# Kernel tuning notes

Measured on AMD Instinct MI355X. Metric: run time of the kernel, lower is better.

## Reference

```python
import jax, jax.numpy as jnp
import numpy as np

B, CIN, H, W = 32, 256, 32, 32
DK, DV, HEADS, OUT = 128, 128, 8, 256
DKH = DK // HEADS
DVH = DV // HEADS


def _conv1x1(x, w, b):
    # x: [B,C,H,W], w: [O,C], b: [O]
    return jnp.einsum('bchw,oc->bohw', x, w) + b[None, :, None, None]


def setup_inputs() -> dict:
    key = jax.random.key(0)
    ks = jax.random.split(key, 7)
    s = 0.02
    return {
        'x': jax.random.normal(ks[0], (B, CIN, H, W), jnp.float32),
        'w_qkv': jax.random.normal(ks[1], (2 * DK + DV, CIN), jnp.float32) * s,
        'b_qkv': jnp.zeros((2 * DK + DV,), jnp.float32),
        'w_attn': jax.random.normal(ks[2], (DV, DV), jnp.float32) * s,
        'b_attn': jnp.zeros((DV,), jnp.float32),
        'w_out': jax.random.normal(ks[3], (OUT - DV, CIN), jnp.float32) * s,
        'b_out': jnp.zeros((OUT - DV,), jnp.float32),
    }


def reference(x, w_qkv, b_qkv, w_attn, b_attn, w_out, b_out):
    b = x.shape[0]
    N = H * W
    # parallel conv branch (kernel_size=1 so spatial dims match attention branch)
    conv_out = _conv1x1(x, w_out, b_out)  # [B, OUT-DV, H, W]
    # qkv projection
    qkv = _conv1x1(x, w_qkv, b_qkv)  # [B, 2*DK+DV, H, W]
    q, k, v = jnp.split(qkv, [DK, 2 * DK], axis=1)
    q = q.reshape(b, HEADS, DKH, N) * (DKH ** -0.5)
    k = k.reshape(b, HEADS, DKH, N)
    v = v.reshape(b, HEADS, DVH, N)
    # scaled dot-product attention over the N=H*W flattened positions
    logits = jnp.einsum('bhdq,bhdk->bhqk', q, k)  # [B,heads,N,N]
    weights = jax.nn.softmax(logits, axis=-1)
    attn = jnp.einsum('bhqk,bhdk->bhdq', weights, v)  # [B,heads,DVH,N]
    attn = attn.reshape(b, DV, H, W)
    attn = _conv1x1(attn, w_attn, b_attn)
    return jnp.concatenate([conv_out, attn], axis=1)
```

## Files before the change

### kernel.cpp

```cpp
#include <hip/hip_runtime.h>
#include <hip/hip_bf16.h>

#define BATCH 32
#define CIN   256
#define NPOS  1024
#define DKC   128
#define DVC   128
#define HEADS 8
#define OUTC  256

typedef __bf16 bf16x8 __attribute__((ext_vector_type(8)));
typedef __bf16 bf16x4 __attribute__((ext_vector_type(4)));
typedef float  f32x4  __attribute__((ext_vector_type(4)));
typedef float  f32x16 __attribute__((ext_vector_type(16)));
typedef unsigned u32x4 __attribute__((ext_vector_type(4)));
typedef unsigned short u16x8 __attribute__((ext_vector_type(8)));

#define QSCALE 0.3606737602f

__device__ inline bf16x8 load8(const __bf16* p) {
    return *reinterpret_cast<const bf16x8*>(p);
}
__device__ inline f32x4 fzero4() {
    f32x4 z;
#pragma unroll
    for (int i = 0; i < 4; ++i) z[i] = 0.0f;
    return z;
}
__device__ inline float fexp2(float x) {
#if __has_builtin(__builtin_amdgcn_exp2f)
    return __builtin_amdgcn_exp2f(x);
#else
    return exp2f(x);
#endif
}

__global__ __launch_bounds__(1024) void detect_dtype(const unsigned short* __restrict__ xraw,
                                                     int* __restrict__ flag) {
    __shared__ int s;
    if (threadIdx.x == 0) s = 0;
    __syncthreads();
    int cnt = 0;
#pragma unroll
    for (int r = 0; r < 4; ++r) {
        u16x8 v = *reinterpret_cast<const u16x8*>(xraw + ((size_t)r * 1024 + threadIdx.x) * 8);
#pragma unroll
        for (int j = 0; j < 8; ++j) {
            unsigned int e = (v[j] >> 7) & 0xFF;
            if (e >= 0x92) cnt++;
        }
    }
    if (cnt) atomicAdd(&s, cnt);
    __syncthreads();
    if (threadIdx.x == 0) *flag = (s > 0) ? 1 : 0;
}

#define CV_WQKV 98304
#define CV_WOUT (CV_WQKV + 32768)
#define CV_BQKV (CV_WOUT + 384)
#define CV_BOUT (CV_BQKV + 128)
#define CV_WATT (CV_BOUT + 16384)
#define CV_BATT (CV_WATT + 128)
__global__ __launch_bounds__(256) void convert_all(
    const void* __restrict__ w_qkv, const void* __restrict__ b_qkv,
    const void* __restrict__ w_attn, const void* __restrict__ b_attn,
    const void* __restrict__ w_out, const void* __restrict__ b_out,
    __bf16* __restrict__ wcat, __bf16* __restrict__ bcat,
    __bf16* __restrict__ w_attnc, __bf16* __restrict__ b_attnc,
    const int* __restrict__ flag) {
    int i = blockIdx.x * 256 + threadIdx.x;
    const void* src; __bf16* dst; int j;
    if      (i < CV_WQKV) { src = w_qkv;  j = i;           dst = wcat + i; }
    else if (i < CV_WOUT) { src = w_out;  j = i - CV_WQKV; dst = wcat + i; }
    else if (i < CV_BQKV) { src = b_qkv;  j = i - CV_WOUT; dst = bcat + j; }
    else if (i < CV_BOUT) { src = b_out;  j = i - CV_BQKV; dst = bcat + 384 + j; }
    else if (i < CV_WATT) { src = w_attn; j = i - CV_BOUT; dst = w_attnc + j; }
    else if (i < CV_BATT) { src = b_attn; j = i - CV_WATT; dst = b_attnc + j; }
    else return;
    if (*flag) *dst = (__bf16)((const float*)src)[j];
    else       *dst = ((const __bf16*)src)[j];
}

__global__ __launch_bounds__(512, 4) void qkv_conv_gemm3(
    const void* __restrict__ xv,
    const __bf16* __restrict__ wcat,
    const __bf16* __restrict__ bcat,
    __bf16* __restrict__ q_ws,
    __bf16* __restrict__ k_ws,
    __bf16* __restrict__ v_ws,
    void* __restrict__ out,
    const int* __restrict__ flag)
{
    __shared__ __bf16 xs[64][264];
    bool isf32 = (*flag != 0);
    int b   = blockIdx.y;
    int n0  = blockIdx.x * 64;
    int t   = threadIdx.x;
    int nl  = t & 63, cb = t >> 6;

#pragma unroll
    for (int cs = 0; cs < 32; ++cs) {
        int c = cs * 8 + cb;
        size_t gi = ((size_t)b * CIN + c) * NPOS + n0 + nl;
        float v = isf32 ? ((const float*)xv)[gi] : (float)((const __bf16*)xv)[gi];
        xs[nl][c] = (__bf16)v;
    }
    __syncthreads();

    int wave = t >> 6;
    int lane = t & 63;
    int quad = lane >> 4, colid = lane & 15;
    int row0 = (wave >> 2) * 256 + (wave & 3) * 64;

    const __bf16* wp = wcat + (size_t)(row0 + colid) * CIN + quad * 8;

    f32x4 acc[4][4];
#pragma unroll
    for (int rt = 0; rt < 4; ++rt)
#pragma unroll
        for (int st = 0; st < 4; ++st) acc[rt][st] = fzero4();

#pragma unroll
    for (int k0 = 0; k0 < CIN; k0 += 32) {
        bf16x8 aA[4], bB[4];
#pragma unroll
        for (int rt = 0; rt < 4; ++rt)
            aA[rt] = load8(wp + (size_t)(rt * 16) * CIN + k0);
#pragma unroll
        for (int st = 0; st < 4; ++st)
            bB[st] = *reinterpret_cast<const bf16x8*>(&xs[st * 16 + colid][k0 + quad * 8]);
#pragma unroll
        for (int rt = 0; rt < 4; ++rt)
#pragma unroll
            for (int st = 0; st < 4; ++st)
                acc[rt][st] = __builtin_amdgcn_mfma_f32_16x16x32_bf16(aA[rt], bB[st], acc[rt][st], 0, 0, 0);
    }

#pragma unroll
    for (int rt = 0; rt < 4; ++rt) {
        int obase = row0 + rt * 16;
        float bias[4];
#pragma unroll
        for (int r = 0; r < 4; ++r) bias[r] = (float)bcat[obase + quad * 4 + r];

        if (obase < DKC) {
            int h = obase >> 4;
            __bf16* qb = q_ws + (((size_t)b * HEADS + h) * NPOS + n0) * 16 + quad * 4;
#pragma unroll
            for (int st = 0; st < 4; ++st) {
                bf16x4 ov;
#pragma unroll
                for (int r = 0; r < 4; ++r)
                    ov[r] = (__bf16)((acc[rt][st][r] + bias[r]) * QSCALE);
                *reinterpret_cast<bf16x4*>(qb + (size_t)(st * 16 + colid) * 16) = ov;
            }
        } else if (obase < 2 * DKC) {
            int h = (obase - DKC) >> 4;
            __bf16* kb = k_ws + (((size_t)b * HEADS + h) * NPOS + n0) * 16 + quad * 4;
#pragma unroll
            for (int st = 0; st < 4; ++st) {
                bf16x4 ov;
#pragma unroll
                for (int r = 0; r < 4; ++r)
                    ov[r] = (__bf16)(acc[rt][st][r] + bias[r]);
                *reinterpret_cast<bf16x4*>(kb + (size_t)(st * 16 + colid) * 16) = ov;
            }
        } else if (obase < 384) {
            int h = (obase - 2 * DKC) >> 4;
            __bf16* vb = v_ws + (((size_t)b * HEADS + h) * 16 + quad * 4) * NPOS + n0 + colid;
#pragma unroll
            for (int r = 0; r < 4; ++r)
#pragma unroll
                for (int st = 0; st < 4; ++st)
                    vb[(size_t)r * NPOS + st * 16] = (__bf16)(acc[rt][st][r] + bias[r]);
        } else {
            int oc = obase - 384 + quad * 4;
#pragma unroll
            for (int r = 0; r < 4; ++r) {
                size_t ob = ((size_t)b * OUTC + oc + r) * NPOS + n0 + colid;
#pragma unroll
                for (int st = 0; st < 4; ++st) {
                    float v = acc[rt][st][r] + bias[r];
                    if (isf32) __builtin_nontemporal_store(v, (float*)out + ob + st * 16);
                    else       __builtin_nontemporal_store((__bf16)v, (__bf16*)out + ob + st * 16);
                }
            }
        }
    }
}

#define OSTR 136
__global__ __launch_bounds__(512, 4) void attention_kernel(
    const __bf16* __restrict__ q_ws,
    const __bf16* __restrict__ k_ws,
    const __bf16* __restrict__ v_ws,
    const __bf16* __restrict__ w_attn,
    const __bf16* __restrict__ b_attn,
    void* __restrict__ out,
    const int* __restrict__ flag)
{
    __shared__ __align__(16) __bf16 olds[64][OSTR];
    int b    = blockIdx.x;
    int nq0  = blockIdx.y * 64;
    int wave = threadIdx.x >> 6;
    int lane = threadIdx.x & 63;
    int l5   = lane & 31, hi = lane >> 5;
    int h    = wave;
    int bh   = b * HEADS + h;

    const __bf16* qp = q_ws + (size_t)bh * NPOS * 16;
    const __bf16* kp = k_ws + (size_t)bh * NPOS * 16;
    const __bf16* vp = v_ws + (size_t)bh * 16 * NPOS;

    bf16x8 qB0 = load8(qp + (size_t)(nq0 + l5) * 16 + hi * 8);
    bf16x8 qB1 = load8(qp + (size_t)(nq0 + 32 + l5) * 16 + hi * 8);

    bf16x8 vA0, vA1;
#pragma unroll
    for (int i = 0; i < 8; ++i) { vA0[i] = (__bf16)1.0f; vA1[i] = (__bf16)1.0f; }
    const __bf16* vrow = vp + (size_t)l5 * NPOS + hi * 8;

    f32x16 zero16;
#pragma unroll
    for (int i = 0; i < 16; ++i) zero16[i] = 0.0f;
    f32x16 acc0 = zero16, acc1 = zero16;

    bf16x8 kA = load8(kp + (size_t)l5 * 16 + hi * 8);
    if (l5 < 16) {
        vA0 = load8(vrow);
        vA1 = load8(vrow + 16);
    }

#pragma unroll 2
    for (int nk0 = 0; nk0 < NPOS; nk0 += 32) {
        int nkn = (nk0 + 32) & (NPOS - 1);
        bf16x8 kA_n = load8(kp + (size_t)(nkn + l5) * 16 + hi * 8);
        bf16x8 vA0_n = vA0, vA1_n = vA1;
        if (l5 < 16) {
            vA0_n = load8(vrow + nkn);
            vA1_n = load8(vrow + nkn + 16);
        }
#pragma unroll
        for (int half = 0; half < 2; ++half) {
            f32x16 st = __builtin_amdgcn_mfma_f32_32x32x16_bf16(
                kA, half ? qB1 : qB0, zero16, 0, 0, 0);
            unsigned w[8];
#pragma unroll
            for (int m = 0; m < 4; ++m) {
                float e0 = fexp2(st[4 * m + 0]);
                float e1 = fexp2(st[4 * m + 1]);
                float e2 = fexp2(st[4 * m + 2]);
                float e3 = fexp2(st[4 * m + 3]);
                unsigned lo, hw;
                asm("v_cvt_pk_bf16_f32 %0, %1, %2" : "=v"(lo) : "v"(e0), "v"(e1));
                asm("v_cvt_pk_bf16_f32 %0, %1, %2" : "=v"(hw) : "v"(e2), "v"(e3));
                w[2 * m]     = lo;
                w[2 * m + 1] = hw;
            }
            asm("v_permlane32_swap_b32 %0, %1" : "+v"(w[0]), "+v"(w[2]));
            asm("v_permlane32_swap_b32 %0, %1" : "+v"(w[1]), "+v"(w[3]));
            asm("v_permlane32_swap_b32 %0, %1" : "+v"(w[4]), "+v"(w[6]));
            asm("v_permlane32_swap_b32 %0, %1" : "+v"(w[5]), "+v"(w[7]));
            u32x4 t1 = {w[0], w[1], w[2], w[3]};
            u32x4 t2 = {w[4], w[5], w[6], w[7]};
            bf16x8 pB1 = __builtin_bit_cast(bf16x8, t1);
            bf16x8 pB2 = __builtin_bit_cast(bf16x8, t2);
            if (half) {
                acc1 = __builtin_amdgcn_mfma_f32_32x32x16_bf16(vA0, pB1, acc1, 0, 0, 0);
                acc1 = __builtin_amdgcn_mfma_f32_32x32x16_bf16(vA1, pB2, acc1, 0, 0, 0);
            } else {
                acc0 = __builtin_amdgcn_mfma_f32_32x32x16_bf16(vA0, pB1, acc0, 0, 0, 0);
                acc0 = __builtin_amdgcn_mfma_f32_32x32x16_bf16(vA1, pB2, acc0, 0, 0, 0);
            }
        }
        kA = kA_n; vA0 = vA0_n; vA1 = vA1_n;
    }
#pragma unroll
    for (int half = 0; half < 2; ++half) {
        const f32x16& acc = half ? acc1 : acc0;
        float inv = 1.0f / acc[8];
        bf16x4 o0, o1;
#pragma unroll
        for (int r = 0; r < 4; ++r) {
            o0[r] = (__bf16)(acc[r] * inv);
            o1[r] = (__bf16)(acc[4 + r] * inv);
        }
        __bf16* ol = &olds[32 * half + l5][h * 16 + 4 * hi];
        *reinterpret_cast<bf16x4*>(ol)     = o0;
        *reinterpret_cast<bf16x4*>(ol + 8) = o1;
    }
    __syncthreads();

    int quad = lane >> 4, colid = lane & 15;
    int row0 = h * 16;
    f32x4 pacc[4];
#pragma unroll
    for (int st = 0; st < 4; ++st) pacc[st] = fzero4();
#pragma unroll
    for (int k0 = 0; k0 < DVC; k0 += 32) {
        bf16x8 a = load8(w_attn + (size_t)(row0 + colid) * DVC + k0 + quad * 8);
#pragma unroll
        for (int st = 0; st < 4; ++st) {
            bf16x8 bb = *reinterpret_cast<const bf16x8*>(&olds[st * 16 + colid][k0 + quad * 8]);
            pacc[st] = __builtin_amdgcn_mfma_f32_16x16x32_bf16(a, bb, pacc[st], 0, 0, 0);
        }
    }
    bool isf32 = (*flag != 0);
#pragma unroll
    for (int r = 0; r < 4; ++r) {
        int o = row0 + quad * 4 + r;
        float bias = (float)b_attn[o];
#pragma unroll
        for (int st = 0; st < 4; ++st) {
            int n = nq0 + st * 16 + colid;
            float v = pacc[st][r] + bias;
            size_t oi = ((size_t)b * OUTC + DVC + o) * NPOS + n;
            if (isf32) __builtin_nontemporal_store(v, (float*)out + oi);
            else       __builtin_nontemporal_store((__bf16)v, (__bf16*)out + oi);
        }
    }
}

extern "C" void kernel_launch(void* const* d_in, const int* in_sizes, int n_in,
                              void* d_out, int out_size, void* d_ws, size_t ws_size,
                              hipStream_t stream) {
    const void* x      = d_in[0];
    const void* w_qkv  = d_in[1];
    const void* b_qkv  = d_in[2];
    const void* w_attn = d_in[3];
    const void* b_attn = d_in[4];
    const void* w_out  = d_in[5];
    const void* b_out  = d_in[6];

    char* ws = (char*)d_ws;
    int*    flag    = (int*)ws;
    __bf16* wcat    = (__bf16*)(ws + (1u << 20));
    __bf16* bcat    = (__bf16*)(ws + (3u << 19));
    __bf16* w_attnc = (__bf16*)(ws + (7u << 18));
    __bf16* b_attnc = (__bf16*)(ws + (1u << 21));
    __bf16* q_ws    = (__bf16*)(ws + (28u << 20));
    __bf16* k_ws    = (__bf16*)(ws + (36u << 20));
    __bf16* v_ws    = (__bf16*)(ws + (44u << 20));

    detect_dtype<<<1, 1024, 0, stream>>>((const unsigned short*)x, flag);
    convert_all<<<(CV_BATT + 255) / 256, 256, 0, stream>>>(
        w_qkv, b_qkv, w_attn, b_attn, w_out, b_out,
        wcat, bcat, w_attnc, b_attnc, flag);

    qkv_conv_gemm3<<<dim3(NPOS / 64, BATCH), 512, 0, stream>>>(
        x, wcat, bcat, q_ws, k_ws, v_ws, d_out, flag);
    attention_kernel<<<dim3(BATCH, NPOS / 64), 512, 0, stream>>>(
        q_ws, k_ws, v_ws, w_attnc, b_attnc, d_out, flag);
}
```

Baseline: 158.2 us.

## Fuse QKV projection and attention into one kernel with per-batch spin barrier

Merges the QKV/conv GEMM kernel and the attention kernel into a single launch of 512 blocks. Each block signals completion of its projection tile on a per-batch atomic counter and spins until all 16 tiles of that batch are done, then runs attention. The separate dtype-detection kernel is dropped and detection moves into convert_all, which samples w_qkv instead of x and resets the counters. This removes two kernel launches and the launch gap between stages. In exchange it relies on all 512 blocks being co-resident to avoid deadlock, and the dtype heuristic now reads the small weights rather than the input.

```diff
diff --git a/kernel.cpp b/kernel.cpp
--- a/kernel.cpp
+++ b/kernel.cpp
@@ -14,7 +14,6 @@
 typedef float  f32x4  __attribute__((ext_vector_type(4)));
 typedef float  f32x16 __attribute__((ext_vector_type(16)));
 typedef unsigned u32x4 __attribute__((ext_vector_type(4)));
-typedef unsigned short u16x8 __attribute__((ext_vector_type(8)));
 
 #define QSCALE 0.3606737602f
 
@@ -33,26 +32,6 @@
 #else
     return exp2f(x);
 #endif
-}
-
-__global__ __launch_bounds__(1024) void detect_dtype(const unsigned short* __restrict__ xraw,
-                                                     int* __restrict__ flag) {
-    __shared__ int s;
-    if (threadIdx.x == 0) s = 0;
-    __syncthreads();
-    int cnt = 0;
-#pragma unroll
-    for (int r = 0; r < 4; ++r) {
-        u16x8 v = *reinterpret_cast<const u16x8*>(xraw + ((size_t)r * 1024 + threadIdx.x) * 8);
-#pragma unroll
-        for (int j = 0; j < 8; ++j) {
-            unsigned int e = (v[j] >> 7) & 0xFF;
-            if (e >= 0x92) cnt++;
-        }
-    }
-    if (cnt) atomicAdd(&s, cnt);
-    __syncthreads();
-    if (threadIdx.x == 0) *flag = (s > 0) ? 1 : 0;
 }
 
 #define CV_WQKV 98304
@@ -67,7 +46,19 @@
     const void* __restrict__ w_out, const void* __restrict__ b_out,
     __bf16* __restrict__ wcat, __bf16* __restrict__ bcat,
     __bf16* __restrict__ w_attnc, __bf16* __restrict__ b_attnc,
-    const int* __restrict__ flag) {
+    int* __restrict__ flag, int* __restrict__ counters) {
+    __shared__ int s;
+    if (threadIdx.x == 0) s = 0;
+    __syncthreads();
+    unsigned short u = ((const unsigned short*)w_qkv)[threadIdx.x];
+    if (((u >> 7) & 0xFF) >= 0x92) atomicAdd(&s, 1);
+    __syncthreads();
+    bool isf32 = (s > 0);
+    if (blockIdx.x == 0) {
+        if (threadIdx.x == 0) *flag = isf32 ? 1 : 0;
+        if (threadIdx.x < BATCH) counters[threadIdx.x] = 0;
+    }
+
     int i = blockIdx.x * 256 + threadIdx.x;
     const void* src; __bf16* dst; int j;
     if      (i < CV_WQKV) { src = w_qkv;  j = i;           dst = wcat + i; }
@@ -77,136 +68,142 @@
     else if (i < CV_WATT) { src = w_attn; j = i - CV_BOUT; dst = w_attnc + j; }
     else if (i < CV_BATT) { src = b_attn; j = i - CV_WATT; dst = b_attnc + j; }
     else return;
-    if (*flag) *dst = (__bf16)((const float*)src)[j];
+    if (isf32) *dst = (__bf16)((const float*)src)[j];
     else       *dst = ((const __bf16*)src)[j];
 }
 
-__global__ __launch_bounds__(512, 4) void qkv_conv_gemm3(
+#define OSTR 136
+__global__ __launch_bounds__(512, 4) void fused_qkv_attn(
     const void* __restrict__ xv,
     const __bf16* __restrict__ wcat,
     const __bf16* __restrict__ bcat,
+    const __bf16* __restrict__ w_attn,
+    const __bf16* __restrict__ b_attn,
     __bf16* __restrict__ q_ws,
     __bf16* __restrict__ k_ws,
     __bf16* __restrict__ v_ws,
     void* __restrict__ out,
-    const int* __restrict__ flag)
+    const int* __restrict__ flag,
+    int* __restrict__ counters)
 {
-    __shared__ __bf16 xs[64][264];
+    __shared__ __align__(16) char smem[64 * 264 * 2];
+    __bf16 (*xs)[264]  = reinterpret_cast<__bf16(*)[264]>(smem);
+    __bf16 (*olds)[OSTR] = reinterpret_cast<__bf16(*)[OSTR]>(smem);
+
     bool isf32 = (*flag != 0);
-    int b   = blockIdx.y;
-    int n0  = blockIdx.x * 64;
+    int id  = blockIdx.x;
+    int b   = id & 31;
+    int n0  = (id >> 5) * 64;
     int t   = threadIdx.x;
-    int nl  = t & 63, cb = t >> 6;
-
-#pragma unroll
-    for (int cs = 0; cs < 32; ++cs) {
-        int c = cs * 8 + cb;
-        size_t gi = ((size_t)b * CIN + c) * NPOS + n0 + nl;
-        float v = isf32 ? ((const float*)xv)[gi] : (float)((const __bf16*)xv)[gi];
-        xs[nl][c] = (__bf16)v;
+
+    {
+        int nl = t & 63, cb = t >> 6;
+#pragma unroll
+        for (int cs = 0; cs < 32; ++cs) {
+            int c = cs * 8 + cb;
+            size_t gi = ((size_t)b * CIN + c) * NPOS + n0 + nl;
+            float v = isf32 ? ((const float*)xv)[gi] : (float)((const __bf16*)xv)[gi];
+            xs[nl][c] = (__bf16)v;
+        }
     }
     __syncthreads();
 
     int wave = t >> 6;
     int lane = t & 63;
     int quad = lane >> 4, colid = lane & 15;
-    int row0 = (wave >> 2) * 256 + (wave & 3) * 64;
-
-    const __bf16* wp = wcat + (size_t)(row0 + colid) * CIN + quad * 8;
-
-    f32x4 acc[4][4];
-#pragma unroll
-    for (int rt = 0; rt < 4; ++rt)
-#pragma unroll
-        for (int st = 0; st < 4; ++st) acc[rt][st] = fzero4();
-
-#pragma unroll
-    for (int k0 = 0; k0 < CIN; k0 += 32) {
-        bf16x8 aA[4], bB[4];
+    {
+        int row0 = (wave >> 2) * 256 + (wave & 3) * 64;
+        const __bf16* wp = wcat + (size_t)(row0 + colid) * CIN + quad * 8;
+
+        f32x4 acc[4][4];
 #pragma unroll
         for (int rt = 0; rt < 4; ++rt)
-            aA[rt] = load8(wp + (size_t)(rt * 16) * CIN + k0);
-#pragma unroll
-        for (int st = 0; st < 4; ++st)
-            bB[st] = *reinterpret_cast<const bf16x8*>(&xs[st * 16 + colid][k0 + quad * 8]);
-#pragma unroll
-        for (int rt = 0; rt < 4; ++rt)
+#pragma unroll
+            for (int st = 0; st < 4; ++st) acc[rt][st] = fzero4();
+
+#pragma unroll
+        for (int k0 = 0; k0 < CIN; k0 += 32) {
+            bf16x8 aA[4], bB[4];
+#pragma unroll
+            for (int rt = 0; rt < 4; ++rt)
+                aA[rt] = load8(wp + (size_t)(rt * 16) * CIN + k0);
 #pragma unroll
             for (int st = 0; st < 4; ++st)
-                acc[rt][st] = __builtin_amdgcn_mfma_f32_16x16x32_bf16(aA[rt], bB[st], acc[rt][st], 0, 0, 0);
-    }
-
-#pragma unroll
-    for (int rt = 0; rt < 4; ++rt) {
-        int obase = row0 + rt * 16;
-        float bias[4];
-#pragma unroll
-        for (int r = 0; r < 4; ++r) bias[r] = (float)bcat[obase + quad * 4 + r];
-
-        if (obase < DKC) {
-            int h = obase >> 4;
-            __bf16* qb = q_ws + (((size_t)b * HEADS + h) * NPOS + n0) * 16 + quad * 4;
-#pragma unroll
-            for (int st = 0; st < 4; ++st) {
-                bf16x4 ov;
+                bB[st] = *reinterpret_cast<const bf16x8*>(&xs[st * 16 + colid][k0 + quad * 8]);
+#pragma unroll
+            for (int rt = 0; rt < 4; ++rt)
+#pragma unroll
+                for (int st = 0; st < 4; ++st)
+                    acc[rt][st] = __builtin_amdgcn_mfma_f32_16x16x32_bf16(aA[rt], bB[st], acc[rt][st], 0, 0, 0);
+        }
+
+#pragma unroll
+        for (int rt = 0; rt < 4; ++rt) {
+            int obase = row0 + rt * 16;
+            float bias[4];
+#pragma unroll
+            for (int r = 0; r < 4; ++r) bias[r] = (float)bcat[obase + quad * 4 + r];
+
+            if (obase < DKC) {
+                int h = obase >> 4;
+                __bf16* qb = q_ws + (((size_t)b * HEADS + h) * NPOS + n0) * 16 + quad * 4;
+#pragma unroll
+                for (int st = 0; st < 4; ++st) {
+                    bf16x4 ov;
+#pragma unroll
+                    for (int r = 0; r < 4; ++r)
+                        ov[r] = (__bf16)((acc[rt][st][r] + bias[r]) * QSCALE);
+                    *reinterpret_cast<bf16x4*>(qb + (size_t)(st * 16 + colid) * 16) = ov;
+                }
+            } else if (obase < 2 * DKC) {
+                int h = (obase - DKC) >> 4;
+                __bf16* kb = k_ws + (((size_t)b * HEADS + h) * NPOS + n0) * 16 + quad * 4;
+#pragma unroll
+                for (int st = 0; st < 4; ++st) {
+                    bf16x4 ov;
+#pragma unroll
+                    for (int r = 0; r < 4; ++r)
+                        ov[r] = (__bf16)(acc[rt][st][r] + bias[r]);
+                    *reinterpret_cast<bf16x4*>(kb + (size_t)(st * 16 + colid) * 16) = ov;
+                }
+            } else if (obase < 384) {
+                int h = (obase - 2 * DKC) >> 4;
+                __bf16* vb = v_ws + (((size_t)b * HEADS + h) * 16 + quad * 4) * NPOS + n0 + colid;
 #pragma unroll
                 for (int r = 0; r < 4; ++r)
-                    ov[r] = (__bf16)((acc[rt][st][r] + bias[r]) * QSCALE);
-                *reinterpret_cast<bf16x4*>(qb + (size_t)(st * 16 + colid) * 16) = ov;
-            }
-        } else if (obase < 2 * DKC) {
-            int h = (obase - DKC) >> 4;
-            __bf16* kb = k_ws + (((size_t)b * HEADS + h) * NPOS + n0) * 16 + quad * 4;
-#pragma unroll
-            for (int st = 0; st < 4; ++st) {
-                bf16x4 ov;
-#pragma unroll
-                for (int r = 0; r < 4; ++r)
-                    ov[r] = (__bf16)(acc[rt][st][r] + bias[r]);
-                *reinterpret_cast<bf16x4*>(kb + (size_t)(st * 16 + colid) * 16) = ov;
-            }
-        } else if (obase < 384) {
-            int h = (obase - 2 * DKC) >> 4;
-            __bf16* vb = v_ws + (((size_t)b * HEADS + h) * 16 + quad * 4) * NPOS + n0 + colid;
-#pragma unroll
-            for (int r = 0; r < 4; ++r)
-#pragma unroll
-                for (int st = 0; st < 4; ++st)
-                    vb[(size_t)r * NPOS + st * 16] = (__bf16)(acc[rt][st][r] + bias[r]);
-        } else {
-            int oc = obase - 384 + quad * 4;
-#pragma unroll
-            for (int r = 0; r < 4; ++r) {
-                size_t ob = ((size_t)b * OUTC + oc + r) * NPOS + n0 + colid;
-#pragma unroll
-                for (int st = 0; st < 4; ++st) {
-                    float v = acc[rt][st][r] + bias[r];
-                    if (isf32) __builtin_nontemporal_store(v, (float*)out + ob + st * 16);
-                    else       __builtin_nontemporal_store((__bf16)v, (__bf16*)out + ob + st * 16);
+#pragma unroll
+                    for (int st = 0; st < 4; ++st)
+                        vb[(size_t)r * NPOS + st * 16] = (__bf16)(acc[rt][st][r] + bias[r]);
+            } else {
+                int oc = obase - 384 + quad * 4;
+#pragma unroll
+                for (int r = 0; r < 4; ++r) {
+                    size_t ob = ((size_t)b * OUTC + oc + r) * NPOS + n0 + colid;
+#pragma unroll
+                    for (int st = 0; st < 4; ++st) {
+                        float v = acc[rt][st][r] + bias[r];
+                        if (isf32) __builtin_nontemporal_store(v, (float*)out + ob + st * 16);
+                        else       __builtin_nontemporal_store((__bf16)v, (__bf16*)out + ob + st * 16);
+                    }
                 }
             }
         }
     }
-}
-
-#define OSTR 136
-__global__ __launch_bounds__(512, 4) void attention_kernel(
-    const __bf16* __restrict__ q_ws,
-    const __bf16* __restrict__ k_ws,
-    const __bf16* __restrict__ v_ws,
-    const __bf16* __restrict__ w_attn,
-    const __bf16* __restrict__ b_attn,
-    void* __restrict__ out,
-    const int* __restrict__ flag)
-{
-    __shared__ __align__(16) __bf16 olds[64][OSTR];
-    int b    = blockIdx.x;
-    int nq0  = blockIdx.y * 64;
-    int wave = threadIdx.x >> 6;
-    int lane = threadIdx.x & 63;
-    int l5   = lane & 31, hi = lane >> 5;
-    int h    = wave;
-    int bh   = b * HEADS + h;
+
+    __syncthreads();
+    if (t == 0) {
+        __hip_atomic_fetch_add(&counters[b], 1, __ATOMIC_RELEASE,
+                               __HIP_MEMORY_SCOPE_AGENT);
+        while (__hip_atomic_load(&counters[b], __ATOMIC_ACQUIRE,
+                                 __HIP_MEMORY_SCOPE_AGENT) < 16)
+            __builtin_amdgcn_s_sleep(2);
+    }
+    __syncthreads();
+
+    int nq0 = n0;
+    int h   = wave;
+    int bh  = b * HEADS + h;
+    int l5  = lane & 31, hi = lane >> 5;
 
     const __bf16* qp = q_ws + (size_t)bh * NPOS * 16;
     const __bf16* kp = k_ws + (size_t)bh * NPOS * 16;
@@ -291,32 +288,32 @@
     }
     __syncthreads();
 
-    int quad = lane >> 4, colid = lane & 15;
-    int row0 = h * 16;
-    f32x4 pacc[4];
-#pragma unroll
-    for (int st = 0; st < 4; ++st) pacc[st] = fzero4();
-#pragma unroll
-    for (int k0 = 0; k0 < DVC; k0 += 32) {
-        bf16x8 a = load8(w_attn + (size_t)(row0 + colid) * DVC + k0 + quad * 8);
-#pragma unroll
-        for (int st = 0; st < 4; ++st) {
-            bf16x8 bb = *reinterpret_cast<const bf16x8*>(&olds[st * 16 + colid][k0 + quad * 8]);
-            pacc[st] = __builtin_amdgcn_mfma_f32_16x16x32_bf16(a, bb, pacc[st], 0, 0, 0);
-        }
-    }
-    bool isf32 = (*flag != 0);
-#pragma unroll
-    for (int r = 0; r < 4; ++r) {
-        int o = row0 + quad * 4 + r;
-        float bias = (float)b_attn[o];
-#pragma unroll
-        for (int st = 0; st < 4; ++st) {
-            int n = nq0 + st * 16 + colid;
-            float v = pacc[st][r] + bias;
-            size_t oi = ((size_t)b * OUTC + DVC + o) * NPOS + n;
-            if (isf32) __builtin_nontemporal_store(v, (float*)out + oi);
-            else       __builtin_nontemporal_store((__bf16)v, (__bf16*)out + oi);
+    {
+        int row0 = h * 16;
+        f32x4 pacc[4];
+#pragma unroll
+        for (int st = 0; st < 4; ++st) pacc[st] = fzero4();
+#pragma unroll
+        for (int k0 = 0; k0 < DVC; k0 += 32) {
+            bf16x8 a = load8(w_attn + (size_t)(row0 + colid) * DVC + k0 + quad * 8);
+#pragma unroll
+            for (int st = 0; st < 4; ++st) {
+                bf16x8 bb = *reinterpret_cast<const bf16x8*>(&olds[st * 16 + colid][k0 + quad * 8]);
+                pacc[st] = __builtin_amdgcn_mfma_f32_16x16x32_bf16(a, bb, pacc[st], 0, 0, 0);
+            }
+        }
+#pragma unroll
+        for (int r = 0; r < 4; ++r) {
+            int o = row0 + quad * 4 + r;
+            float bias = (float)b_attn[o];
+#pragma unroll
+            for (int st = 0; st < 4; ++st) {
+                int n = nq0 + st * 16 + colid;
+                float v = pacc[st][r] + bias;
+                size_t oi = ((size_t)b * OUTC + DVC + o) * NPOS + n;
+                if (isf32) __builtin_nontemporal_store(v, (float*)out + oi);
+                else       __builtin_nontemporal_store((__bf16)v, (__bf16*)out + oi);
+            }
         }
     }
 }
@@ -333,22 +330,20 @@
     const void* b_out  = d_in[6];
 
     char* ws = (char*)d_ws;
-    int*    flag    = (int*)ws;
-    __bf16* wcat    = (__bf16*)(ws + (1u << 20));
-    __bf16* bcat    = (__bf16*)(ws + (3u << 19));
-    __bf16* w_attnc = (__bf16*)(ws + (7u << 18));
-    __bf16* b_attnc = (__bf16*)(ws + (1u << 21));
-    __bf16* q_ws    = (__bf16*)(ws + (28u << 20));
-    __bf16* k_ws    = (__bf16*)(ws + (36u << 20));
-    __bf16* v_ws    = (__bf16*)(ws + (44u << 20));
-
-    detect_dtype<<<1, 1024, 0, stream>>>((const unsigned short*)x, flag);
+    int*    flag     = (int*)ws;
+    int*    counters = (int*)(ws + 256);
+    __bf16* wcat     = (__bf16*)(ws + (1u << 20));
+    __bf16* bcat     = (__bf16*)(ws + (3u << 19));
+    __bf16* w_attnc  = (__bf16*)(ws + (7u << 18));
+    __bf16* b_attnc  = (__bf16*)(ws + (1u << 21));
+    __bf16* q_ws     = (__bf16*)(ws + (28u << 20));
+    __bf16* k_ws     = (__bf16*)(ws + (36u << 20));
+    __bf16* v_ws     = (__bf16*)(ws + (44u << 20));
+
     convert_all<<<(CV_BATT + 255) / 256, 256, 0, stream>>>(
         w_qkv, b_qkv, w_attn, b_attn, w_out, b_out,
-        wcat, bcat, w_attnc, b_attnc, flag);
-
-    qkv_conv_gemm3<<<dim3(NPOS / 64, BATCH), 512, 0, stream>>>(
-        x, wcat, bcat, q_ws, k_ws, v_ws, d_out, flag);
-    attention_kernel<<<dim3(BATCH, NPOS / 64), 512, 0, stream>>>(
-        q_ws, k_ws, v_ws, w_attnc, b_attnc, d_out, flag);
-}
+        wcat, bcat, w_attnc, b_attnc, flag, counters);
+
+    fused_qkv_attn<<<dim3(512), 512, 0, stream>>>(
+        x, wcat, bcat, w_attnc, b_attnc, q_ws, k_ws, v_ws, d_out, flag, counters);
+}
```

New measurement: 189.6 us. 1.2x slower.
